# Kernel tuning notes

Hardware: AMD Instinct MI355X
Metric: run time of the kernel (lower is better)

The kernel has to match this reference:

```python
import jax, jax.numpy as jnp
import numpy as np

HIDDEN = 512
HEADS = 8
HEAD_DIM = HIDDEN // HEADS


def setup_inputs() -> dict:
    key = jax.random.key(0)
    ks = jax.random.split(key, 12)
    B, S = 2, 2048
    s = 1.0 / np.sqrt(HIDDEN)
    inp = {
        "query": jax.random.normal(ks[0], (B, S, HIDDEN), dtype=jnp.float32),
        "key": jax.random.normal(ks[1], (B, S, HIDDEN), dtype=jnp.float32),
        "value": jax.random.normal(ks[2], (B, S, HIDDEN), dtype=jnp.float32),
        "Wq": jax.random.uniform(ks[3], (HIDDEN, HIDDEN), jnp.float32, -s, s),
        "bq": jnp.zeros((HIDDEN,), jnp.float32),
        "Wk": jax.random.uniform(ks[4], (HIDDEN, HIDDEN), jnp.float32, -s, s),
        "bk": jnp.zeros((HIDDEN,), jnp.float32),
        "Wv": jax.random.uniform(ks[5], (HIDDEN, HIDDEN), jnp.float32, -s, s),
        "bv": jnp.zeros((HIDDEN,), jnp.float32),
        "Wo": jax.random.uniform(ks[6], (HIDDEN, HIDDEN), jnp.float32, -s, s),
        "bo": jnp.zeros((HIDDEN,), jnp.float32),
    }
    return inp


def reference(query, key, value, Wq, bq, Wk, bk, Wv, bv, Wo, bo):
    B, S, _ = query.shape
    scale = jnp.sqrt(jnp.asarray(HEAD_DIM, dtype=query.dtype))
    # Linear projections (torch Linear: x @ W.T + b)
    Q = (query @ Wq.T + bq).reshape(B, S, HEADS, HEAD_DIM).transpose(0, 2, 1, 3)
    K = (key @ Wk.T + bk).reshape(B, S, HEADS, HEAD_DIM).transpose(0, 2, 1, 3)
    V = (value @ Wv.T + bv).reshape(B, S, HEADS, HEAD_DIM).transpose(0, 2, 1, 3)
    # Scores: [B, H, S, S]
    energy = jnp.einsum("bhqd,bhkd->bhqk", Q, K) / scale
    attn = jax.nn.softmax(energy, axis=-1)
    # Dropout is identity in eval mode.
    x = jnp.einsum("bhqk,bhkd->bhqd", attn, V)
    x = x.transpose(0, 2, 1, 3).reshape(B, S, HIDDEN)
    return x @ Wo.T + bo
```

## Files before the change

kernel.cpp:

```cpp
#include <hip/hip_runtime.h>

typedef __bf16 bf16x8 __attribute__((ext_vector_type(8)));
typedef float f32x4 __attribute__((ext_vector_type(4)));
typedef unsigned int uint4v __attribute__((ext_vector_type(4)));

__device__ __forceinline__ unsigned short f2bf(float f) {
  union { float f; unsigned int u; } v; v.f = f;
  unsigned int u = v.u;
  u += 0x7FFFu + ((u >> 16) & 1u);
  return (unsigned short)(u >> 16);
}

__device__ __forceinline__ unsigned int pack2bf(float a, float b) {
  return (unsigned int)f2bf(a) | ((unsigned int)f2bf(b) << 16);
}

__global__ __launch_bounds__(256) void convert_w(
    const float* wq, const float* wk, const float* wv, const float* wo,
    unsigned short* wqc, unsigned short* wkc, unsigned short* wvc,
    unsigned short* woc, float qscale)
{
  const float* src; unsigned short* dst; float sc = 1.f;
  switch (blockIdx.y) {
    case 0: src = wq; dst = wqc; sc = qscale; break;
    case 1: src = wk; dst = wkc; break;
    case 2: src = wv; dst = wvc; break;
    default: src = wo; dst = woc; break;
  }
  int idx = (blockIdx.x * 256 + threadIdx.x) * 8;
  f32x4 a = *(const f32x4*)(src + idx);
  f32x4 b = *(const f32x4*)(src + idx + 4);
  uint4v p;
  p.x = pack2bf(a.x * sc, a.y * sc);
  p.y = pack2bf(a.z * sc, a.w * sc);
  p.z = pack2bf(b.x * sc, b.y * sc);
  p.w = pack2bf(b.z * sc, b.w * sc);
  *(uint4v*)(dst + idx) = p;
}

template<int OUT, bool AF32>
__device__ __forceinline__ void gemm_core(
    const void* __restrict__ Ap, const unsigned short* __restrict__ W,
    const float* __restrict__ bias, void* __restrict__ Cp,
    float bscale, int mbase, int nbase)
{
  __shared__ union {
    struct { unsigned short As[64][40]; unsigned short Bs[128][40]; } t;
    unsigned short Cs[128][72];
  } u;

  const int tid  = threadIdx.x;
  const int wave = tid >> 6, lane = tid & 63;
  const int lrow = lane & 15, lgrp = lane >> 4;
  const int ar = tid >> 2, ac = (tid & 3) * 8;

  const unsigned short* Bg0 = W + (size_t)(nbase + ar) * 512 + ac;
  const unsigned short* Bg1 = W + (size_t)(nbase + ar + 64) * 512 + ac;

  f32x4 acc[4][2];
#pragma unroll
  for (int i = 0; i < 4; i++)
#pragma unroll
    for (int j = 0; j < 2; j++) acc[i][j] = (f32x4){0.f, 0.f, 0.f, 0.f};

  const unsigned short* Ab = (const unsigned short*)Ap;
  const float*          Af = (const float*)Ap;
  uint4v pA; f32x4 pAf0, pAf1;
  if constexpr (AF32) {
    const float* base = Af + (size_t)(mbase + ar) * 512 + ac;
    pAf0 = *(const f32x4*)(base);
    pAf1 = *(const f32x4*)(base + 4);
  } else {
    pA = *(const uint4v*)(Ab + (size_t)(mbase + ar) * 512 + ac);
  }
  uint4v pB0 = *(const uint4v*)Bg0;
  uint4v pB1 = *(const uint4v*)Bg1;

  for (int kt = 0; kt < 512; kt += 32) {
    __syncthreads();
    if constexpr (AF32) {
      uint4v w;
      w.x = pack2bf(pAf0.x, pAf0.y); w.y = pack2bf(pAf0.z, pAf0.w);
      w.z = pack2bf(pAf1.x, pAf1.y); w.w = pack2bf(pAf1.z, pAf1.w);
      *(uint4v*)&u.t.As[ar][ac] = w;
    } else {
      *(uint4v*)&u.t.As[ar][ac] = pA;
    }
    *(uint4v*)&u.t.Bs[ar][ac]      = pB0;
    *(uint4v*)&u.t.Bs[ar + 64][ac] = pB1;
    __syncthreads();
    if (kt + 32 < 512) {
      if constexpr (AF32) {
        const float* base = Af + (size_t)(mbase + ar) * 512 + ac + kt + 32;
        pAf0 = *(const f32x4*)(base);
        pAf1 = *(const f32x4*)(base + 4);
      } else {
        pA = *(const uint4v*)(Ab + (size_t)(mbase + ar) * 512 + ac + kt + 32);
      }
      pB0 = *(const uint4v*)(Bg0 + kt + 32);
      pB1 = *(const uint4v*)(Bg1 + kt + 32);
    }
    bf16x8 a[4], b[2];
#pragma unroll
    for (int mi = 0; mi < 4; mi++)
      a[mi] = *(const bf16x8*)&u.t.As[mi * 16 + lrow][lgrp * 8];
#pragma unroll
    for (int ni = 0; ni < 2; ni++)
      b[ni] = *(const bf16x8*)&u.t.Bs[wave * 32 + ni * 16 + lrow][lgrp * 8];
#pragma unroll
    for (int mi = 0; mi < 4; mi++)
#pragma unroll
      for (int ni = 0; ni < 2; ni++)
        acc[mi][ni] = __builtin_amdgcn_mfma_f32_16x16x32_bf16(
            a[mi], b[ni], acc[mi][ni], 0, 0, 0);
  }

  if constexpr (OUT == 2) {
    __syncthreads();
#pragma unroll
    for (int ni = 0; ni < 2; ni++) {
      int col_l = wave * 32 + ni * 16 + lrow;
      float bv = bias[nbase + col_l];
#pragma unroll
      for (int mi = 0; mi < 4; mi++) {
        int row_l = mi * 16 + lgrp * 4;
#pragma unroll
        for (int r = 0; r < 4; r++)
          u.Cs[col_l][row_l + r] = f2bf(acc[mi][ni][r] + bv);
      }
    }
    __syncthreads();
    const int bb = mbase >> 11, s_base = mbase & 2047;
    unsigned short* Vt = (unsigned short*)Cp;
#pragma unroll
    for (int ks = 0; ks < 4; ks++) {
      int seg = tid + ks * 256;
      int c = seg >> 3, r0 = (seg & 7) * 8;
      uint4v val = *(const uint4v*)&u.Cs[c][r0];
      int n = nbase + c, hh = n >> 6, d = n & 63;
      *(uint4v*)(Vt + ((size_t)(bb * 8 + hh) * 64 + d) * 2048 + s_base + r0) = val;
    }
  } else {
#pragma unroll
    for (int ni = 0; ni < 2; ni++) {
      int col = nbase + wave * 32 + ni * 16 + lrow;
      float bv = bias[col] * bscale;
#pragma unroll
      for (int mi = 0; mi < 4; mi++) {
        int row0 = mbase + mi * 16 + lgrp * 4;
#pragma unroll
        for (int r = 0; r < 4; r++) {
          float val = acc[mi][ni][r] + bv;
          if constexpr (OUT == 0)
            ((unsigned short*)Cp)[(size_t)(row0 + r) * 512 + col] = f2bf(val);
          else
            ((float*)Cp)[(size_t)(row0 + r) * 512 + col] = val;
        }
      }
    }
  }
}

__global__ __launch_bounds__(256) void qkv_gemm(
    const float* q, const float* k, const float* v,
    const unsigned short* wqc, const unsigned short* wkc,
    const unsigned short* wvc,
    const float* bq, const float* bk, const float* bv,
    unsigned short* Qb, unsigned short* Kb, unsigned short* Vt, float qscale)
{
  const int z = blockIdx.z;
  const int mb = blockIdx.y * 64, nb = blockIdx.x * 128;
  if (z == 2)      gemm_core<2, true>(v, wvc, bv, Vt, 1.f, mb, nb);
  else if (z == 0) gemm_core<0, true>(q, wqc, bq, Qb, qscale, mb, nb);
  else             gemm_core<0, true>(k, wkc, bk, Kb, 1.f, mb, nb);
}

__global__ __launch_bounds__(256) void out_gemm(
    const unsigned short* ctx, const unsigned short* woc,
    const float* bo, float* out)
{
  gemm_core<1, false>(ctx, woc, bo, out, 1.f, blockIdx.y * 64, blockIdx.x * 128);
}

__global__ __launch_bounds__(256) void attn_kernel(
    const unsigned short* Qb, const unsigned short* Kb,
    const unsigned short* Vt, unsigned short* ctx)
{
  __shared__ unsigned short Ks[128][74];
  __shared__ unsigned short Vs[64][134];
  __shared__ unsigned short Ps[128][134];

  const int tid  = threadIdx.x;
  const int wave = tid >> 6, lane = tid & 63;
  const int lrow = lane & 15, lgrp = lane >> 4;
  const int bh = blockIdx.y, b = bh >> 3, h = bh & 7;
  const int qbase = blockIdx.x * 128;

  const unsigned short* Qg  = Qb + (size_t)(b * 2048 + qbase) * 512 + h * 64;
  const unsigned short* Kg  = Kb + (size_t)(b * 2048) * 512 + h * 64;
  const unsigned short* Vtg = Vt + (size_t)bh * 64 * 2048;

#pragma unroll
  for (int i = 0; i < 4; i++) {
    int seg = tid + i * 256;
    int row = seg >> 3, c0 = (seg & 7) * 8;
    *(uint4v*)&Ps[row][c0] = *(const uint4v*)(Qg + (size_t)row * 512 + c0);
  }
  __syncthreads();
  bf16x8 qf[2][2];
#pragma unroll
  for (int mi = 0; mi < 2; mi++)
#pragma unroll
    for (int kh = 0; kh < 2; kh++)
      qf[mi][kh] = *(const bf16x8*)&Ps[wave * 32 + mi * 16 + lrow][kh * 32 + lgrp * 8];

  const int s0  = tid >> 3, kc_ = (tid & 7) * 8;
  const int krow0 = ((s0 & 15) << 3) | (s0 >> 4);
  const int vd_ = tid >> 4, vc_ = (tid & 15) * 8;

  float lst[2][4] = {{0.f,0.f,0.f,0.f},{0.f,0.f,0.f,0.f}};
  f32x4 oacc[2][4];
#pragma unroll
  for (int mi = 0; mi < 2; mi++)
#pragma unroll
    for (int d = 0; d < 4; d++) oacc[mi][d] = (f32x4){0.f, 0.f, 0.f, 0.f};

  uint4v kr[4], vr[4];
#pragma unroll
  for (int i = 0; i < 4; i++) {
    kr[i] = *(const uint4v*)(Kg + (size_t)(krow0 + 2 * i) * 512 + kc_);
    vr[i] = *(const uint4v*)(Vtg + (size_t)(vd_ + 16 * i) * 2048 + vc_);
  }

  for (int it = 0; it < 16; ++it) {
    __syncthreads();
#pragma unroll
    for (int i = 0; i < 4; i++) {
      *(uint4v*)&Ks[s0 + 32 * i][kc_]  = kr[i];
      *(uint4v*)&Vs[vd_ + 16 * i][vc_] = vr[i];
    }
    __syncthreads();
    if (it < 15) {
      const int key0 = (it + 1) * 128;
#pragma unroll
      for (int i = 0; i < 4; i++) {
        kr[i] = *(const uint4v*)(Kg + (size_t)(key0 + krow0 + 2 * i) * 512 + kc_);
        vr[i] = *(const uint4v*)(Vtg + (size_t)(vd_ + 16 * i) * 2048 + key0 + vc_);
      }
    }

    f32x4 sacc[2][8];
#pragma unroll
    for (int mi = 0; mi < 2; mi++)
#pragma unroll
      for (int ni = 0; ni < 8; ni++) sacc[mi][ni] = (f32x4){0.f, 0.f, 0.f, 0.f};
#pragma unroll
    for (int ni = 0; ni < 8; ni++) {
      bf16x8 k0 = *(const bf16x8*)&Ks[ni * 16 + lrow][lgrp * 8];
      bf16x8 k1 = *(const bf16x8*)&Ks[ni * 16 + lrow][32 + lgrp * 8];
#pragma unroll
      for (int mi = 0; mi < 2; mi++) {
        sacc[mi][ni] = __builtin_amdgcn_mfma_f32_16x16x32_bf16(qf[mi][0], k0, sacc[mi][ni], 0, 0, 0);
        sacc[mi][ni] = __builtin_amdgcn_mfma_f32_16x16x32_bf16(qf[mi][1], k1, sacc[mi][ni], 0, 0, 0);
      }
    }

#pragma unroll
    for (int mi = 0; mi < 2; mi++)
#pragma unroll
      for (int ni = 0; ni < 8; ni++)
#pragma unroll
        for (int r = 0; r < 4; r++) {
          float p = exp2f(sacc[mi][ni][r]);
          sacc[mi][ni][r] = p;
          lst[mi][r] += p;
        }

#pragma unroll
    for (int mi = 0; mi < 2; mi++)
#pragma unroll
      for (int r = 0; r < 4; r++) {
        uint4v pk;
        pk.x = pack2bf(sacc[mi][0][r], sacc[mi][1][r]);
        pk.y = pack2bf(sacc[mi][2][r], sacc[mi][3][r]);
        pk.z = pack2bf(sacc[mi][4][r], sacc[mi][5][r]);
        pk.w = pack2bf(sacc[mi][6][r], sacc[mi][7][r]);
        *(uint4v*)&Ps[wave * 32 + mi * 16 + lgrp * 4 + r][lrow * 8] = pk;
      }

#pragma unroll
    for (int ks = 0; ks < 4; ks++) {
      bf16x8 pa[2];
#pragma unroll
      for (int mi = 0; mi < 2; mi++)
        pa[mi] = *(const bf16x8*)&Ps[wave * 32 + mi * 16 + lrow][ks * 32 + lgrp * 8];
#pragma unroll
      for (int dt = 0; dt < 4; dt++) {
        bf16x8 vb = *(const bf16x8*)&Vs[dt * 16 + lrow][ks * 32 + lgrp * 8];
#pragma unroll
        for (int mi = 0; mi < 2; mi++)
          oacc[mi][dt] = __builtin_amdgcn_mfma_f32_16x16x32_bf16(pa[mi], vb, oacc[mi][dt], 0, 0, 0);
      }
    }
  }

#pragma unroll
  for (int m = 1; m < 16; m <<= 1)
#pragma unroll
    for (int mi = 0; mi < 2; mi++)
#pragma unroll
      for (int r = 0; r < 4; r++) lst[mi][r] += __shfl_xor(lst[mi][r], m, 64);

  unsigned short* Cg = ctx + (size_t)(b * 2048 + qbase) * 512 + h * 64;
#pragma unroll
  for (int mi = 0; mi < 2; mi++) {
    float inv[4];
#pragma unroll
    for (int r = 0; r < 4; r++) inv[r] = 1.0f / lst[mi][r];
#pragma unroll
    for (int dt = 0; dt < 4; dt++)
#pragma unroll
      for (int r = 0; r < 4; r++) {
        int row = wave * 32 + mi * 16 + lgrp * 4 + r;
        int col = dt * 16 + lrow;
        Cg[(size_t)row * 512 + col] = f2bf(oacc[mi][dt][r] * inv[r]);
      }
  }
}

extern "C" void kernel_launch(void* const* d_in, const int* in_sizes, int n_in,
                              void* d_out, int out_size, void* d_ws, size_t ws_size,
                              hipStream_t stream)
{
  const float* q  = (const float*)d_in[0];
  const float* k  = (const float*)d_in[1];
  const float* v  = (const float*)d_in[2];
  const float* Wq = (const float*)d_in[3];
  const float* bq = (const float*)d_in[4];
  const float* Wk = (const float*)d_in[5];
  const float* bk = (const float*)d_in[6];
  const float* Wv = (const float*)d_in[7];
  const float* bv = (const float*)d_in[8];
  const float* Wo = (const float*)d_in[9];
  const float* bo = (const float*)d_in[10];
  float* out = (float*)d_out;

  unsigned short* wqc = (unsigned short*)d_ws;
  unsigned short* wkc = wqc + (1 << 18);
  unsigned short* wvc = wkc + (1 << 18);
  unsigned short* woc = wvc + (1 << 18);
  unsigned short* Qb  = woc + (1 << 18);
  unsigned short* Kb  = Qb  + (1 << 21);
  unsigned short* Vt  = Kb  + (1 << 21);
  unsigned short* Cb  = Vt  + (1 << 21);

  const float qscale = 0.125f * 1.44269504088896340736f;

  convert_w<<<dim3(128, 4), 256, 0, stream>>>(
      Wq, Wk, Wv, Wo, wqc, wkc, wvc, woc, qscale);
  qkv_gemm<<<dim3(4, 64, 3), 256, 0, stream>>>(
      q, k, v, wqc, wkc, wvc, bq, bk, bv, Qb, Kb, Vt, qscale);
  attn_kernel<<<dim3(16, 16), 256, 0, stream>>>(Qb, Kb, Vt, Cb);
  out_gemm<<<dim3(4, 64), 256, 0, stream>>>(Cb, woc, bo, out);
}
```

Measured before the change: 169.8 us.

## Split attention key tiles across wave pairs and halve query tile per block

New measurement: 159.8 us. -5.9%, faster.

```diff
diff --git a/kernel.cpp b/kernel.cpp
--- a/kernel.cpp
+++ b/kernel.cpp
@@ -3,6 +3,7 @@
 typedef __bf16 bf16x8 __attribute__((ext_vector_type(8)));
 typedef float f32x4 __attribute__((ext_vector_type(4)));
 typedef unsigned int uint4v __attribute__((ext_vector_type(4)));
+typedef unsigned int uint2v __attribute__((ext_vector_type(2)));
 
 __device__ __forceinline__ unsigned short f2bf(float f) {
   union { float f; unsigned int u; } v; v.f = f;
@@ -187,36 +188,37 @@
     const unsigned short* Vt, unsigned short* ctx)
 {
   __shared__ unsigned short Ks[128][74];
-  __shared__ unsigned short Vs[64][134];
-  __shared__ unsigned short Ps[128][134];
+  __shared__ unsigned short Vs[64][140];
+  __shared__ unsigned short Ps[2][64][76];
 
   const int tid  = threadIdx.x;
   const int wave = tid >> 6, lane = tid & 63;
   const int lrow = lane & 15, lgrp = lane >> 4;
+  const int qh = wave >> 1, kh = wave & 1;
   const int bh = blockIdx.y, b = bh >> 3, h = bh & 7;
-  const int qbase = blockIdx.x * 128;
+  const int qbase = blockIdx.x * 64;
 
   const unsigned short* Qg  = Qb + (size_t)(b * 2048 + qbase) * 512 + h * 64;
   const unsigned short* Kg  = Kb + (size_t)(b * 2048) * 512 + h * 64;
   const unsigned short* Vtg = Vt + (size_t)bh * 64 * 2048;
 
 #pragma unroll
-  for (int i = 0; i < 4; i++) {
+  for (int i = 0; i < 2; i++) {
     int seg = tid + i * 256;
     int row = seg >> 3, c0 = (seg & 7) * 8;
-    *(uint4v*)&Ps[row][c0] = *(const uint4v*)(Qg + (size_t)row * 512 + c0);
+    *(uint4v*)&Ps[0][row][c0] = *(const uint4v*)(Qg + (size_t)row * 512 + c0);
   }
   __syncthreads();
   bf16x8 qf[2][2];
 #pragma unroll
   for (int mi = 0; mi < 2; mi++)
 #pragma unroll
-    for (int kh = 0; kh < 2; kh++)
-      qf[mi][kh] = *(const bf16x8*)&Ps[wave * 32 + mi * 16 + lrow][kh * 32 + lgrp * 8];
-
-  const int s0  = tid >> 3, kc_ = (tid & 7) * 8;
+    for (int c = 0; c < 2; c++)
+      qf[mi][c] = *(const bf16x8*)&Ps[0][qh * 32 + mi * 16 + lrow][c * 32 + lgrp * 8];
+
+  const int s0 = tid >> 3, kc_ = (tid & 7) * 8;
   const int krow0 = ((s0 & 15) << 3) | (s0 >> 4);
-  const int vd_ = tid >> 4, vc_ = (tid & 15) * 8;
+  const int vd_ = tid >> 4, vcl = (tid & 15);
 
   float lst[2][4] = {{0.f,0.f,0.f,0.f},{0.f,0.f,0.f,0.f}};
   f32x4 oacc[2][4];
@@ -229,15 +231,16 @@
 #pragma unroll
   for (int i = 0; i < 4; i++) {
     kr[i] = *(const uint4v*)(Kg + (size_t)(krow0 + 2 * i) * 512 + kc_);
-    vr[i] = *(const uint4v*)(Vtg + (size_t)(vd_ + 16 * i) * 2048 + vc_);
+    vr[i] = *(const uint4v*)(Vtg + (size_t)(vd_ + 16 * i) * 2048 + vcl * 8);
   }
 
   for (int it = 0; it < 16; ++it) {
     __syncthreads();
 #pragma unroll
     for (int i = 0; i < 4; i++) {
-      *(uint4v*)&Ks[s0 + 32 * i][kc_]  = kr[i];
-      *(uint4v*)&Vs[vd_ + 16 * i][vc_] = vr[i];
+      *(uint4v*)&Ks[s0 + 32 * i][kc_] = kr[i];
+      *(uint2v*)&Vs[vd_ + 16 * i][vcl * 4]      = (uint2v){vr[i].x, vr[i].y};
+      *(uint2v*)&Vs[vd_ + 16 * i][64 + vcl * 4] = (uint2v){vr[i].z, vr[i].w};
     }
     __syncthreads();
     if (it < 15) {
@@ -245,19 +248,20 @@
 #pragma unroll
       for (int i = 0; i < 4; i++) {
         kr[i] = *(const uint4v*)(Kg + (size_t)(key0 + krow0 + 2 * i) * 512 + kc_);
-        vr[i] = *(const uint4v*)(Vtg + (size_t)(vd_ + 16 * i) * 2048 + key0 + vc_);
-      }
-    }
-
-    f32x4 sacc[2][8];
-#pragma unroll
-    for (int mi = 0; mi < 2; mi++)
-#pragma unroll
-      for (int ni = 0; ni < 8; ni++) sacc[mi][ni] = (f32x4){0.f, 0.f, 0.f, 0.f};
-#pragma unroll
-    for (int ni = 0; ni < 8; ni++) {
-      bf16x8 k0 = *(const bf16x8*)&Ks[ni * 16 + lrow][lgrp * 8];
-      bf16x8 k1 = *(const bf16x8*)&Ks[ni * 16 + lrow][32 + lgrp * 8];
+        vr[i] = *(const uint4v*)(Vtg + (size_t)(vd_ + 16 * i) * 2048 + key0 + vcl * 8);
+      }
+    }
+
+    f32x4 sacc[2][4];
+#pragma unroll
+    for (int mi = 0; mi < 2; mi++)
+#pragma unroll
+      for (int ni = 0; ni < 4; ni++) sacc[mi][ni] = (f32x4){0.f, 0.f, 0.f, 0.f};
+#pragma unroll
+    for (int ni = 0; ni < 4; ni++) {
+      const int t = 4 * kh + ni;
+      bf16x8 k0 = *(const bf16x8*)&Ks[t * 16 + lrow][lgrp * 8];
+      bf16x8 k1 = *(const bf16x8*)&Ks[t * 16 + lrow][32 + lgrp * 8];
 #pragma unroll
       for (int mi = 0; mi < 2; mi++) {
         sacc[mi][ni] = __builtin_amdgcn_mfma_f32_16x16x32_bf16(qf[mi][0], k0, sacc[mi][ni], 0, 0, 0);
@@ -268,7 +272,7 @@
 #pragma unroll
     for (int mi = 0; mi < 2; mi++)
 #pragma unroll
-      for (int ni = 0; ni < 8; ni++)
+      for (int ni = 0; ni < 4; ni++)
 #pragma unroll
         for (int r = 0; r < 4; r++) {
           float p = exp2f(sacc[mi][ni][r]);
@@ -280,23 +284,21 @@
     for (int mi = 0; mi < 2; mi++)
 #pragma unroll
       for (int r = 0; r < 4; r++) {
-        uint4v pk;
+        uint2v pk;
         pk.x = pack2bf(sacc[mi][0][r], sacc[mi][1][r]);
         pk.y = pack2bf(sacc[mi][2][r], sacc[mi][3][r]);
-        pk.z = pack2bf(sacc[mi][4][r], sacc[mi][5][r]);
-        pk.w = pack2bf(sacc[mi][6][r], sacc[mi][7][r]);
-        *(uint4v*)&Ps[wave * 32 + mi * 16 + lgrp * 4 + r][lrow * 8] = pk;
-      }
-
-#pragma unroll
-    for (int ks = 0; ks < 4; ks++) {
+        *(uint2v*)&Ps[kh][qh * 32 + mi * 16 + lgrp * 4 + r][lrow * 4] = pk;
+      }
+
+#pragma unroll
+    for (int ks = 0; ks < 2; ks++) {
       bf16x8 pa[2];
 #pragma unroll
       for (int mi = 0; mi < 2; mi++)
-        pa[mi] = *(const bf16x8*)&Ps[wave * 32 + mi * 16 + lrow][ks * 32 + lgrp * 8];
+        pa[mi] = *(const bf16x8*)&Ps[kh][qh * 32 + mi * 16 + lrow][ks * 32 + lgrp * 8];
 #pragma unroll
       for (int dt = 0; dt < 4; dt++) {
-        bf16x8 vb = *(const bf16x8*)&Vs[dt * 16 + lrow][ks * 32 + lgrp * 8];
+        bf16x8 vb = *(const bf16x8*)&Vs[dt * 16 + lrow][kh * 64 + ks * 32 + lgrp * 8];
 #pragma unroll
         for (int mi = 0; mi < 2; mi++)
           oacc[mi][dt] = __builtin_amdgcn_mfma_f32_16x16x32_bf16(pa[mi], vb, oacc[mi][dt], 0, 0, 0);
@@ -311,19 +313,35 @@
 #pragma unroll
       for (int r = 0; r < 4; r++) lst[mi][r] += __shfl_xor(lst[mi][r], m, 64);
 
-  unsigned short* Cg = ctx + (size_t)(b * 2048 + qbase) * 512 + h * 64;
-#pragma unroll
-  for (int mi = 0; mi < 2; mi++) {
-    float inv[4];
-#pragma unroll
-    for (int r = 0; r < 4; r++) inv[r] = 1.0f / lst[mi][r];
-#pragma unroll
-    for (int dt = 0; dt < 4; dt++)
+  __syncthreads();
+  float* Obuf = (float*)&Ks[0][0];
+  float* Lbuf = (float*)&Vs[0][0];
+  if (kh == 1) {
+#pragma unroll
+    for (int mi = 0; mi < 2; mi++)
 #pragma unroll
       for (int r = 0; r < 4; r++) {
-        int row = wave * 32 + mi * 16 + lgrp * 4 + r;
-        int col = dt * 16 + lrow;
-        Cg[(size_t)row * 512 + col] = f2bf(oacc[mi][dt][r] * inv[r]);
+        int row = qh * 32 + mi * 16 + lgrp * 4 + r;
+#pragma unroll
+        for (int dt = 0; dt < 4; dt++)
+          Obuf[row * 68 + dt * 16 + lrow] = oacc[mi][dt][r];
+        if (lrow == 0) Lbuf[row] = lst[mi][r];
+      }
+  }
+  __syncthreads();
+  if (kh == 0) {
+    unsigned short* Cg = ctx + (size_t)(b * 2048 + qbase) * 512 + h * 64;
+#pragma unroll
+    for (int mi = 0; mi < 2; mi++)
+#pragma unroll
+      for (int r = 0; r < 4; r++) {
+        int row = qh * 32 + mi * 16 + lgrp * 4 + r;
+        float inv = 1.0f / (lst[mi][r] + Lbuf[row]);
+#pragma unroll
+        for (int dt = 0; dt < 4; dt++) {
+          float val = (oacc[mi][dt][r] + Obuf[row * 68 + dt * 16 + lrow]) * inv;
+          Cg[(size_t)(qbase >= 0 ? row : row) * 512 + dt * 16 + lrow] = f2bf(val);
+        }
       }
   }
 }
@@ -360,6 +378,6 @@
       Wq, Wk, Wv, Wo, wqc, wkc, wvc, woc, qscale);
   qkv_gemm<<<dim3(4, 64, 3), 256, 0, stream>>>(
       q, k, v, wqc, wkc, wvc, bq, bk, bv, Qb, Kb, Vt, qscale);
-  attn_kernel<<<dim3(16, 16), 256, 0, stream>>>(Qb, Kb, Vt, Cb);
+  attn_kernel<<<dim3(32, 16), 256, 0, stream>>>(Qb, Kb, Vt, Cb);
   out_gemm<<<dim3(4, 64), 256, 0, stream>>>(Cb, woc, bo, out);
 }
```
